# Kernel optimization log

Hardware: AMD Instinct MI355X
Metric: run time of the kernel (lower is better)

The kernel has to match this reference:

```python
import jax, jax.numpy as jnp
import numpy as np
import math

D_MODEL = 1024
N_HEADS = 16
D_K = D_MODEL // N_HEADS
MAX_LEN = 200
B, S = 64, 200


def _temporal_bias():
    # bias[i, j] = -0.1 * |i - j| / max_len, same for every head
    idx = jnp.arange(MAX_LEN, dtype=jnp.float32)
    dist = jnp.abs(idx[:, None] - idx[None, :])  # [L, L]
    tb = (-0.1 * dist / MAX_LEN)[None, None, :, :]  # [1, 1, L, L]
    return jnp.broadcast_to(tb, (1, N_HEADS, MAX_LEN, MAX_LEN))


def setup_inputs() -> dict:
    key = jax.random.key(0)
    ks = jax.random.split(key, 9)
    lim = 1.0 / math.sqrt(D_MODEL)
    def lin_w(k):
        return jax.random.uniform(k, (D_MODEL, D_MODEL), jnp.float32, -lim, lim)
    def lin_b(k):
        return jax.random.uniform(k, (D_MODEL,), jnp.float32, -lim, lim)
    return {
        "x": jax.random.normal(ks[0], (B, S, D_MODEL), jnp.float32),
        "mask": jnp.ones((B, 1, S, S), jnp.int32),
        "wq": lin_w(ks[1]), "bq": lin_b(ks[2]),
        "wk": lin_w(ks[3]), "bk": lin_b(ks[4]),
        "wv": lin_w(ks[5]), "bv": lin_b(ks[6]),
        "wo": lin_w(ks[7]), "bo": lin_b(ks[8]),
        "temporal_bias": _temporal_bias(),
    }


def reference(x, mask, wq, bq, wk, bk, wv, bv, wo, bo, temporal_bias):
    b, s, d = x.shape
    h, dk = N_HEADS, D_K
    scale = math.sqrt(dk)
    # torch Linear: y = x @ W.T + b; heads: [b, s, h, dk] -> [b, h, s, dk]
    q = (jnp.einsum('bsd,ed->bse', x, wq) + bq).reshape(b, s, h, dk).transpose(0, 2, 1, 3)
    k = (jnp.einsum('bsd,ed->bse', x, wk) + bk).reshape(b, s, h, dk).transpose(0, 2, 1, 3)
    v = (jnp.einsum('bsd,ed->bse', x, wv) + bv).reshape(b, s, h, dk).transpose(0, 2, 1, 3)
    scores = jnp.einsum('bhqd,bhkd->bhqk', q, k) / scale  # [b, h, s, s]
    scores = scores + temporal_bias[:, :, :s, :s]
    scores = jnp.where(mask == 0, jnp.float32(-1e9), scores)
    attn = jax.nn.softmax(scores, axis=-1)  # dropout is identity in eval mode
    ctx = jnp.einsum('bhqk,bhkd->bhqd', attn, v)
    ctx = ctx.transpose(0, 2, 1, 3).reshape(b, s, d)
    out = jnp.einsum('bsd,ed->bse', ctx, wo) + bo
    return out, attn
```

## Files before the change

kernel.cpp:

```cpp
#include <hip/hip_runtime.h>
#include <stdint.h>

typedef unsigned short u16;
typedef unsigned long long u64;
typedef __bf16 bf16x8 __attribute__((ext_vector_type(8)));
typedef float f32x4 __attribute__((ext_vector_type(4)));

#define MFMA16(a, b, c) __builtin_amdgcn_mfma_f32_16x16x32_bf16((a), (b), (c), 0, 0, 0)

#define BB 64
#define SS 200
#define DM 1024
#define NH 16
#define MM (BB * SS)
#define OUT0_ELEMS (MM * DM)

__device__ static inline u16 f2bf(float f) {
    __bf16 h = (__bf16)f;
    return __builtin_bit_cast(u16, h);
}

__device__ static inline bf16x8 load8(const u16* p) {
    uint4 u = *(const uint4*)p;
    union { uint4 u; bf16x8 b; } cv; cv.u = u; return cv.b;
}

__device__ static inline bf16x8 bzero8() {
    union { uint4 u; bf16x8 b; } cv; cv.u = make_uint4(0u, 0u, 0u, 0u); return cv.b;
}

__device__ static inline void gload_lds16(const void* g, void* l) {
    __builtin_amdgcn_global_load_lds(
        (const __attribute__((address_space(1))) void*)g,
        (__attribute__((address_space(3))) void*)l, 16, 0, 0);
}

__global__ __launch_bounds__(256) void convert_k(
    const float* __restrict__ x,
    const float* __restrict__ wq, const float* __restrict__ wk,
    const float* __restrict__ wv, const float* __restrict__ wo,
    u16* __restrict__ xb,
    u16* __restrict__ wqb, u16* __restrict__ wkb,
    u16* __restrict__ wvb, u16* __restrict__ wob)
{
    size_t i4 = (size_t)blockIdx.x * 256 + threadIdx.x;
    size_t e = i4 * 4;
    const float* src; u16* dst; size_t off;
    if (e < (size_t)OUT0_ELEMS) { src = x; dst = xb; off = e; }
    else {
        size_t we = e - OUT0_ELEMS;
        size_t w = we >> 20;
        off = we & 1048575u;
        src = (w == 0) ? wq : (w == 1) ? wk : (w == 2) ? wv : wo;
        dst = (w == 0) ? wqb : (w == 1) ? wkb : (w == 2) ? wvb : wob;
    }
    float4 v = *(const float4*)(src + off);
    union { u16 s[4]; uint2 u; } o;
    o.s[0] = f2bf(v.x); o.s[1] = f2bf(v.y); o.s[2] = f2bf(v.z); o.s[3] = f2bf(v.w);
    *(uint2*)(dst + off) = o.u;
}

__global__ __launch_bounds__(256) void maskbits_k(
    const int* __restrict__ mask, u64* __restrict__ bits)
{
    __shared__ unsigned char nb[4][64];
    const int wave = threadIdx.x >> 6, lane = threadIdx.x & 63;
    const int row = blockIdx.x * 4 + wave;
    const int* mp = mask + (size_t)row * 200;
    unsigned nib;
    if (lane < 50) {
        int4 v = *(const int4*)(mp + lane * 4);
        nib = (v.x ? 1u : 0u) | (v.y ? 2u : 0u) | (v.z ? 4u : 0u) | (v.w ? 8u : 0u);
    } else nib = 0xFu;
    nb[wave][lane] = (unsigned char)nib;
    __builtin_amdgcn_s_waitcnt(0);
    if (lane < 4) {
        const unsigned char* p = &nb[wave][lane * 16];
        u64 m = 0;
#pragma unroll
        for (int i = 0; i < 16; i++) m |= (u64)(p[i] & 0xFu) << (4 * i);
        bits[(size_t)row * 4 + lane] = m;
    }
}

template <int MODE>
__global__ __launch_bounds__(256) void gemm_k(
    const u16* __restrict__ A, const u16* __restrict__ W,
    const float* __restrict__ b0, const float* __restrict__ b1, const float* __restrict__ b2,
    u16* __restrict__ qo, u16* __restrict__ ko, u16* __restrict__ vto,
    float* __restrict__ outf)
{
    __shared__ __align__(16) u16 sm[8192];
    u16* As = sm;
    u16* Bs = sm + 4096;

    const int tid  = threadIdx.x;
    const int wave = tid >> 6;
    const int lane = tid & 63;
    const int quad = lane >> 4;
    const int l15  = lane & 15;
    const int n0   = blockIdx.x * 128;
    const int m0   = blockIdx.y * 128;
    const int seg  = (MODE == 0) ? (n0 >> 10) : 0;
    const int nn0  = n0 & 1023;
    const float* bias = (MODE == 1) ? b0 : (seg == 0 ? b0 : (seg == 1 ? b1 : b2));

    const int srow = wave * 16 + (lane >> 2);
    const int sk8  = (lane & 3) * 8;
    const int wuni = __builtin_amdgcn_readfirstlane(wave);

    f32x4 acc[4][4];
#pragma unroll
    for (int i = 0; i < 4; i++)
#pragma unroll
        for (int j = 0; j < 4; j++) acc[i][j] = (f32x4){0.f, 0.f, 0.f, 0.f};

    const int wr = (wave >> 1) * 64;
    const int wc = (wave & 1) * 64;

    const u16* Ag = A + (size_t)m0 * 1024;
    const u16* Wg = W + (size_t)n0 * 1024;

    for (int kc = 0; kc < 1024; kc += 32) {
        __syncthreads();
#pragma unroll
        for (int r = 0; r < 2; r++) {
            int row = r * 64 + srow;
            gload_lds16(Ag + (size_t)row * 1024 + kc + sk8, &As[(r * 64 + wuni * 16) * 32]);
        }
#pragma unroll
        for (int r = 0; r < 2; r++) {
            int row = r * 64 + srow;
            gload_lds16(Wg + (size_t)row * 1024 + kc + sk8, &Bs[(r * 64 + wuni * 16) * 32]);
        }
        __syncthreads();

        bf16x8 af[4], bf[4];
#pragma unroll
        for (int mt = 0; mt < 4; mt++) af[mt] = load8(&As[(wr + mt * 16 + l15) * 32 + quad * 8]);
#pragma unroll
        for (int nt = 0; nt < 4; nt++) bf[nt] = load8(&Bs[(wc + nt * 16 + l15) * 32 + quad * 8]);
#pragma unroll
        for (int mt = 0; mt < 4; mt++)
#pragma unroll
            for (int nt = 0; nt < 4; nt++)
                acc[mt][nt] = MFMA16(af[mt], bf[nt], acc[mt][nt]);
    }

    if (MODE == 1) {
#pragma unroll
        for (int nt = 0; nt < 4; nt++) {
            int n = n0 + wc + nt * 16 + l15;
            float bv = bias[n];
#pragma unroll
            for (int mt = 0; mt < 4; mt++)
#pragma unroll
                for (int r = 0; r < 4; r++) {
                    int m = m0 + wr + mt * 16 + quad * 4 + r;
                    outf[(size_t)m * 1024 + n] = acc[mt][nt][r] + bv;
                }
        }
    } else if (seg == 2) {
#pragma unroll
        for (int nt = 0; nt < 4; nt++) {
            int nn = nn0 + wc + nt * 16 + l15;
            float bv = bias[nn];
            int hh = nn >> 6, d = nn & 63;
#pragma unroll
            for (int mt = 0; mt < 4; mt++) {
                int mbase = m0 + wr + mt * 16 + quad * 4;
                int b = mbase / 200, s = mbase - b * 200;
                union { u16 q[4]; uint2 u; } pk;
#pragma unroll
                for (int r = 0; r < 4; r++) pk.q[r] = f2bf(acc[mt][nt][r] + bv);
                *(uint2*)&vto[((size_t)(b * 16 + hh) * 64 + d) * 200 + s] = pk.u;
            }
        }
    } else {
        u16* dst = (seg == 0) ? qo : ko;
        float bv[4];
#pragma unroll
        for (int nt = 0; nt < 4; nt++) bv[nt] = bias[nn0 + wc + nt * 16 + l15];
#pragma unroll
        for (int h2 = 0; h2 < 2; h2++) {
            __syncthreads();
            if ((wave >> 1) == h2) {
#pragma unroll
                for (int nt = 0; nt < 4; nt++)
#pragma unroll
                    for (int mt = 0; mt < 4; mt++)
#pragma unroll
                        for (int r = 0; r < 4; r++) {
                            int rl = mt * 16 + quad * 4 + r;
                            int c  = wc + nt * 16 + l15;
                            sm[rl * 128 + (c ^ ((rl & 7) << 4))] = f2bf(acc[mt][nt][r] + bv[nt]);
                        }
            }
            __syncthreads();
#pragma unroll
            for (int j = 0; j < 4; j++) {
                int idx = tid + j * 256;
                int rl = idx >> 4, c8 = (idx & 15) * 8;
                int c8s = c8 ^ ((rl & 7) << 4);
                uint4 vv = *(const uint4*)&sm[rl * 128 + c8s];
                *(uint4*)&dst[((size_t)(m0 + h2 * 64 + rl)) * 1024 + nn0 + c8] = vv;
            }
        }
    }
}

__global__ __launch_bounds__(256) void attn_k(
    const u16* __restrict__ qg, const u16* __restrict__ kg, const u16* __restrict__ vtg,
    const u64* __restrict__ mbits,
    float* __restrict__ attn_out, u16* __restrict__ ctxb)
{
    __shared__ __align__(16) float Sf[4][16 * 212];

    const int tid  = threadIdx.x;
    const int wave = tid >> 6;
    const int lane = tid & 63;
    const int quad = lane >> 4;
    const int l15  = lane & 15;
    const int bh   = blockIdx.y;
    const int b    = bh >> 4;
    const int h    = bh & 15;
    const int i0   = blockIdx.x * 64 + wave * 16;
    if (i0 >= 200) return;

    float* sf = Sf[wave];
    u16*   pb = (u16*)sf;

    int qi = i0 + l15;
    const u16* qrow = qg + ((size_t)(b * 200 + (qi < 200 ? qi : 0))) * 1024 + h * 64;
    bf16x8 aq0, aq1;
    if (qi < 200) { aq0 = load8(qrow + quad * 8); aq1 = load8(qrow + 32 + quad * 8); }
    else          { aq0 = bzero8(); aq1 = bzero8(); }

#pragma unroll
    for (int t = 0; t < 13; t++) {
        int kj = t * 16 + l15;
        const u16* krow = kg + ((size_t)(b * 200 + (kj < 200 ? kj : 0))) * 1024 + h * 64;
        bf16x8 bk0, bk1;
        if (kj < 200) { bk0 = load8(krow + quad * 8); bk1 = load8(krow + 32 + quad * 8); }
        else          { bk0 = bzero8(); bk1 = bzero8(); }
        f32x4 z = (f32x4){0.f, 0.f, 0.f, 0.f};
        z = MFMA16(aq0, bk0, z);
        z = MFMA16(aq1, bk1, z);
#pragma unroll
        for (int r = 0; r < 4; r++) sf[(quad * 4 + r) * 212 + t * 16 + l15] = z[r];
    }

    const int row = lane >> 2, sub = lane & 3;
    const int iabs = i0 + row;
    const bool rowok = iabs < 200;
    const int irow = rowok ? iabs : 0;
    const u64* mb = mbits + ((size_t)b * 200 + irow) * 4;
    ulonglong2 mA = *(const ulonglong2*)mb;
    ulonglong2 mB = *(const ulonglong2*)(mb + 2);
    const float fi = (float)irow;
    const float TBC = -0.1f / 200.0f;

    f32x4 sv[13];
    float mx = -3.0e38f;
#pragma unroll
    for (int c = 0; c < 13; c++) {
        int col = c * 16 + sub * 4;
        f32x4 s = *(const f32x4*)&sf[row * 212 + col];
        if (rowok && col < 200) {
            u64 ch = (col < 64) ? mA.x : (col < 128) ? mA.y : (col < 192) ? mB.x : mB.y;
            int sh = col & 63;
            s[0] = s[0] * 0.125f + TBC * fabsf(fi - (float)(col + 0));
            s[1] = s[1] * 0.125f + TBC * fabsf(fi - (float)(col + 1));
            s[2] = s[2] * 0.125f + TBC * fabsf(fi - (float)(col + 2));
            s[3] = s[3] * 0.125f + TBC * fabsf(fi - (float)(col + 3));
            if (!((ch >> (sh + 0)) & 1)) s[0] = -1e9f;
            if (!((ch >> (sh + 1)) & 1)) s[1] = -1e9f;
            if (!((ch >> (sh + 2)) & 1)) s[2] = -1e9f;
            if (!((ch >> (sh + 3)) & 1)) s[3] = -1e9f;
        } else { s[0] = s[1] = s[2] = s[3] = -3.0e38f; }
        sv[c] = s;
        mx = fmaxf(mx, fmaxf(fmaxf(s[0], s[1]), fmaxf(s[2], s[3])));
    }
    mx = fmaxf(mx, __shfl_xor(mx, 1, 64));
    mx = fmaxf(mx, __shfl_xor(mx, 2, 64));

    float sum = 0.f;
#pragma unroll
    for (int c = 0; c < 13; c++) {
        f32x4 s = sv[c];
        s[0] = __expf(s[0] - mx); s[1] = __expf(s[1] - mx);
        s[2] = __expf(s[2] - mx); s[3] = __expf(s[3] - mx);
        sv[c] = s;
        sum += (s[0] + s[1]) + (s[2] + s[3]);
    }
    sum += __shfl_xor(sum, 1, 64);
    sum += __shfl_xor(sum, 2, 64);
    float inv = (sum > 0.f) ? 1.f / sum : 0.f;

    float* aop = attn_out + ((size_t)bh * 200 + irow) * 200;
#pragma unroll
    for (int c = 0; c < 13; c++) {
        int col = c * 16 + sub * 4;
        f32x4 a = sv[c];
        a[0] *= inv; a[1] *= inv; a[2] *= inv; a[3] *= inv;
        union { u16 q[4]; uint2 u; } pk;
        if (col < 200) {
            pk.q[0] = f2bf(a[0]); pk.q[1] = f2bf(a[1]);
            pk.q[2] = f2bf(a[2]); pk.q[3] = f2bf(a[3]);
        } else pk.u = make_uint2(0u, 0u);
        *(uint2*)&pb[row * 208 + col] = pk.u;
        if (rowok && col < 200)
            *(float4*)(aop + col) = make_float4(a[0], a[1], a[2], a[3]);
    }

    f32x4 ctx[4];
#pragma unroll
    for (int nt = 0; nt < 4; nt++) ctx[nt] = (f32x4){0.f, 0.f, 0.f, 0.f};
    const u16* vb = vtg + (size_t)bh * 64 * 200;
#pragma unroll
    for (int kc = 0; kc < 224; kc += 32) {
        int j0 = kc + quad * 8;
        bf16x8 af = (j0 < 208) ? load8(pb + l15 * 208 + j0) : bzero8();
#pragma unroll
        for (int nt = 0; nt < 4; nt++) {
            bf16x8 bvf = (j0 < 200) ? load8(vb + (nt * 16 + l15) * 200 + j0) : bzero8();
            ctx[nt] = MFMA16(af, bvf, ctx[nt]);
        }
    }

#pragma unroll
    for (int nt = 0; nt < 4; nt++)
#pragma unroll
        for (int r = 0; r < 4; r++)
            pb[(quad * 4 + r) * 208 + nt * 16 + l15] = f2bf(ctx[nt][r]);

#pragma unroll
    for (int k = 0; k < 2; k++) {
        int rr = k * 8 + (lane >> 3), ss = lane & 7;
        int ia = i0 + rr;
        uint4 val = *(const uint4*)&pb[rr * 208 + ss * 8];
        if (ia < 200)
            *(uint4*)&ctxb[((size_t)b * 200 + ia) * 1024 + h * 64 + ss * 8] = val;
    }
}

extern "C" void kernel_launch(void* const* d_in, const int* in_sizes, int n_in,
                              void* d_out, int out_size, void* d_ws, size_t ws_size,
                              hipStream_t stream) {
    const float* x    = (const float*)d_in[0];
    const int*   mask = (const int*)d_in[1];
    const float* wq   = (const float*)d_in[2];
    const float* bq   = (const float*)d_in[3];
    const float* wk   = (const float*)d_in[4];
    const float* bk   = (const float*)d_in[5];
    const float* wv   = (const float*)d_in[6];
    const float* bv   = (const float*)d_in[7];
    const float* wo   = (const float*)d_in[8];
    const float* bo   = (const float*)d_in[9];

    float* out  = (float*)d_out;
    float* attn = out + OUT0_ELEMS;

    char* ws = (char*)d_ws;
    u16* xb    = (u16*)(ws);
    u16* wqb   = (u16*)(ws + 26214400);
    u16* wkb   = (u16*)(ws + 28311552);
    u16* wvb   = (u16*)(ws + 30408704);
    u16* wob   = (u16*)(ws + 32505856);
    u16* qb    = (u16*)(ws + 34603008);
    u16* kb    = (u16*)(ws + 60817408);
    u16* vtb   = (u16*)(ws + 87031808);
    u16* ctxb  = (u16*)(ws + 113246208);
    u64* mbits = (u64*)(ws + 139460608);

    convert_k<<<dim3(16896), dim3(256), 0, stream>>>(x, wq, wk, wv, wo, xb, wqb, wkb, wvb, wob);

    maskbits_k<<<dim3(3200), dim3(256), 0, stream>>>(mask, mbits);

    gemm_k<0><<<dim3(24, 100), dim3(256), 0, stream>>>(
        xb, wqb, bq, bk, bv, qb, kb, vtb, nullptr);

    attn_k<<<dim3(4, 1024), dim3(256), 0, stream>>>(qb, kb, vtb, mbits, attn, ctxb);

    gemm_k<1><<<dim3(8, 100), dim3(256), 0, stream>>>(
        ctxb, wob, bo, nullptr, nullptr, nullptr, nullptr, nullptr, out);
}
```

Baseline: 551.4 us.

## Compute softmax in MFMA registers, pack attention tasks densely, use nontemporal stores

The attention kernel now applies scale, bias, mask and softmax directly on the MFMA output registers. Row reductions use cross-lane shuffles, so the fp32 score tile no longer round-trips through shared memory, and LDS shrinks to a bf16 probability buffer. Query tiles are packed as 13 per (batch, head), so no waves idle on the padded fourth block. Launch bounds request higher occupancy, and the attention and output stores are nontemporal. The trade-off is that per-element scalar stores replace float4 vector stores for the attention matrix, which may reduce write coalescing.

```diff
diff --git a/kernel.cpp b/kernel.cpp
--- a/kernel.cpp
+++ b/kernel.cpp
@@ -157,7 +157,8 @@
 #pragma unroll
                 for (int r = 0; r < 4; r++) {
                     int m = m0 + wr + mt * 16 + quad * 4 + r;
-                    outf[(size_t)m * 1024 + n] = acc[mt][nt][r] + bv;
+                    __builtin_nontemporal_store(acc[mt][nt][r] + bv,
+                                                &outf[(size_t)m * 1024 + n]);
                 }
         }
     } else if (seg == 2) {
@@ -209,108 +210,113 @@
     }
 }
 
-__global__ __launch_bounds__(256) void attn_k(
+__global__ __launch_bounds__(256, 4) void attn_k(
     const u16* __restrict__ qg, const u16* __restrict__ kg, const u16* __restrict__ vtg,
     const u64* __restrict__ mbits,
     float* __restrict__ attn_out, u16* __restrict__ ctxb)
 {
-    __shared__ __align__(16) float Sf[4][16 * 212];
+    __shared__ __align__(16) u16 Pb[4][16 * 208];
 
     const int tid  = threadIdx.x;
     const int wave = tid >> 6;
     const int lane = tid & 63;
     const int quad = lane >> 4;
     const int l15  = lane & 15;
-    const int bh   = blockIdx.y;
+
+    const int task = blockIdx.x * 4 + wave;
+    const int bh   = task / 13;
+    const int i0   = (task - bh * 13) * 16;
     const int b    = bh >> 4;
     const int h    = bh & 15;
-    const int i0   = blockIdx.x * 64 + wave * 16;
-    if (i0 >= 200) return;
-
-    float* sf = Sf[wave];
-    u16*   pb = (u16*)sf;
-
+
+    u16* pb = Pb[wave];
+
+    const u16* qkbase = qg + (size_t)b * 200 * 1024 + h * 64;
     int qi = i0 + l15;
-    const u16* qrow = qg + ((size_t)(b * 200 + (qi < 200 ? qi : 0))) * 1024 + h * 64;
+    const u16* qrow = qkbase + (size_t)(qi < 200 ? qi : 0) * 1024;
     bf16x8 aq0, aq1;
     if (qi < 200) { aq0 = load8(qrow + quad * 8); aq1 = load8(qrow + 32 + quad * 8); }
     else          { aq0 = bzero8(); aq1 = bzero8(); }
 
+    const int ib = i0 + quad * 4;
+    const u16* kbase = kg + (size_t)b * 200 * 1024 + h * 64;
+    const u64* mrow = mbits + (size_t)b * 200 * 4;
+    const float TBC = -0.1f / 200.0f;
+
+    f32x4 sv[13];
+    f32x4 mxr = (f32x4){-3.0e38f, -3.0e38f, -3.0e38f, -3.0e38f};
+    u64 mw[4];
+
 #pragma unroll
     for (int t = 0; t < 13; t++) {
         int kj = t * 16 + l15;
-        const u16* krow = kg + ((size_t)(b * 200 + (kj < 200 ? kj : 0))) * 1024 + h * 64;
+        const u16* krow = kbase + (size_t)(kj < 200 ? kj : 0) * 1024;
         bf16x8 bk0, bk1;
         if (kj < 200) { bk0 = load8(krow + quad * 8); bk1 = load8(krow + 32 + quad * 8); }
         else          { bk0 = bzero8(); bk1 = bzero8(); }
         f32x4 z = (f32x4){0.f, 0.f, 0.f, 0.f};
         z = MFMA16(aq0, bk0, z);
         z = MFMA16(aq1, bk1, z);
-#pragma unroll
-        for (int r = 0; r < 4; r++) sf[(quad * 4 + r) * 212 + t * 16 + l15] = z[r];
-    }
-
-    const int row = lane >> 2, sub = lane & 3;
-    const int iabs = i0 + row;
-    const bool rowok = iabs < 200;
-    const int irow = rowok ? iabs : 0;
-    const u64* mb = mbits + ((size_t)b * 200 + irow) * 4;
-    ulonglong2 mA = *(const ulonglong2*)mb;
-    ulonglong2 mB = *(const ulonglong2*)(mb + 2);
-    const float fi = (float)irow;
-    const float TBC = -0.1f / 200.0f;
-
-    f32x4 sv[13];
-    float mx = -3.0e38f;
-#pragma unroll
-    for (int c = 0; c < 13; c++) {
-        int col = c * 16 + sub * 4;
-        f32x4 s = *(const f32x4*)&sf[row * 212 + col];
-        if (rowok && col < 200) {
-            u64 ch = (col < 64) ? mA.x : (col < 128) ? mA.y : (col < 192) ? mB.x : mB.y;
-            int sh = col & 63;
-            s[0] = s[0] * 0.125f + TBC * fabsf(fi - (float)(col + 0));
-            s[1] = s[1] * 0.125f + TBC * fabsf(fi - (float)(col + 1));
-            s[2] = s[2] * 0.125f + TBC * fabsf(fi - (float)(col + 2));
-            s[3] = s[3] * 0.125f + TBC * fabsf(fi - (float)(col + 3));
-            if (!((ch >> (sh + 0)) & 1)) s[0] = -1e9f;
-            if (!((ch >> (sh + 1)) & 1)) s[1] = -1e9f;
-            if (!((ch >> (sh + 2)) & 1)) s[2] = -1e9f;
-            if (!((ch >> (sh + 3)) & 1)) s[3] = -1e9f;
-        } else { s[0] = s[1] = s[2] = s[3] = -3.0e38f; }
-        sv[c] = s;
-        mx = fmaxf(mx, fmaxf(fmaxf(s[0], s[1]), fmaxf(s[2], s[3])));
-    }
-    mx = fmaxf(mx, __shfl_xor(mx, 1, 64));
-    mx = fmaxf(mx, __shfl_xor(mx, 2, 64));
-
-    float sum = 0.f;
-#pragma unroll
-    for (int c = 0; c < 13; c++) {
-        f32x4 s = sv[c];
-        s[0] = __expf(s[0] - mx); s[1] = __expf(s[1] - mx);
-        s[2] = __expf(s[2] - mx); s[3] = __expf(s[3] - mx);
-        sv[c] = s;
-        sum += (s[0] + s[1]) + (s[2] + s[3]);
-    }
-    sum += __shfl_xor(sum, 1, 64);
-    sum += __shfl_xor(sum, 2, 64);
-    float inv = (sum > 0.f) ? 1.f / sum : 0.f;
-
-    float* aop = attn_out + ((size_t)bh * 200 + irow) * 200;
-#pragma unroll
-    for (int c = 0; c < 13; c++) {
-        int col = c * 16 + sub * 4;
-        f32x4 a = sv[c];
-        a[0] *= inv; a[1] *= inv; a[2] *= inv; a[3] *= inv;
-        union { u16 q[4]; uint2 u; } pk;
-        if (col < 200) {
-            pk.q[0] = f2bf(a[0]); pk.q[1] = f2bf(a[1]);
-            pk.q[2] = f2bf(a[2]); pk.q[3] = f2bf(a[3]);
-        } else pk.u = make_uint2(0u, 0u);
-        *(uint2*)&pb[row * 208 + col] = pk.u;
-        if (rowok && col < 200)
-            *(float4*)(aop + col) = make_float4(a[0], a[1], a[2], a[3]);
+
+        if ((t & 3) == 0) {
+            const int c = t >> 2;
+#pragma unroll
+            for (int r = 0; r < 4; r++) {
+                int ia = ib + r;
+                mw[r] = mrow[(size_t)(ia < 200 ? ia : 0) * 4 + c];
+            }
+        }
+        const int col = t * 16 + l15;
+        const int sh  = (t & 3) * 16 + l15;
+        const float fc = (float)col;
+        f32x4 s;
+#pragma unroll
+        for (int r = 0; r < 4; r++) {
+            int ia = ib + r;
+            float val = z[r] * 0.125f + TBC * fabsf((float)ia - fc);
+            if (!((mw[r] >> sh) & 1)) val = -1e9f;
+            s[r] = (ia < 200 && col < 200) ? val : -3.0e38f;
+            mxr[r] = fmaxf(mxr[r], s[r]);
+        }
+        sv[t] = s;
+    }
+
+#pragma unroll
+    for (int m = 1; m < 16; m <<= 1)
+#pragma unroll
+        for (int r = 0; r < 4; r++)
+            mxr[r] = fmaxf(mxr[r], __shfl_xor(mxr[r], m, 64));
+
+    f32x4 sum = (f32x4){0.f, 0.f, 0.f, 0.f};
+#pragma unroll
+    for (int t = 0; t < 13; t++) {
+        f32x4 s = sv[t];
+#pragma unroll
+        for (int r = 0; r < 4; r++) { s[r] = __expf(s[r] - mxr[r]); sum[r] += s[r]; }
+        sv[t] = s;
+    }
+#pragma unroll
+    for (int m = 1; m < 16; m <<= 1)
+#pragma unroll
+        for (int r = 0; r < 4; r++)
+            sum[r] += __shfl_xor(sum[r], m, 64);
+
+    f32x4 inv;
+#pragma unroll
+    for (int r = 0; r < 4; r++) inv[r] = (sum[r] > 0.f) ? 1.f / sum[r] : 0.f;
+
+    float* aop = attn_out + (size_t)bh * 40000;
+#pragma unroll
+    for (int t = 0; t < 13; t++) {
+        const int col = t * 16 + l15;
+#pragma unroll
+        for (int r = 0; r < 4; r++) {
+            int ia = ib + r;
+            float a = sv[t][r] * inv[r];
+            pb[(quad * 4 + r) * 208 + col] = (col < 200) ? f2bf(a) : (u16)0;
+            if (ia < 200 && col < 200)
+                __builtin_nontemporal_store(a, aop + (size_t)ia * 200 + col);
+        }
     }
 
     f32x4 ctx[4];
@@ -380,7 +386,7 @@
     gemm_k<0><<<dim3(24, 100), dim3(256), 0, stream>>>(
         xb, wqb, bq, bk, bv, qb, kb, vtb, nullptr);
 
-    attn_k<<<dim3(4, 1024), dim3(256), 0, stream>>>(qb, kb, vtb, mbits, attn, ctxb);
+    attn_k<<<dim3(3328), dim3(256), 0, stream>>>(qb, kb, vtb, mbits, attn, ctxb);
 
     gemm_k<1><<<dim3(8, 100), dim3(256), 0, stream>>>(
         ctxb, wob, bo, nullptr, nullptr, nullptr, nullptr, nullptr, out);
```

Result: slower. 565.2 us (+2.5%).
